# Optimization experiments

Hardware: AMD Instinct MI355X
Metric: run time of the kernel (lower is better)

## Reference

```python
import jax, jax.numpy as jnp
import numpy as np

N_ATOMS = 16384
N_BLOCKS = 4096
K = 3          # top-k nearest context atoms (min(3, n_ctx) in original; n_ctx >> 3 here)
EPS_W = 1e-8   # inverse-distance weight epsilon (matches original)
EPS_D = 1e-12  # tiny epsilon inside sqrt for numerical safety of the distance


def setup_inputs() -> dict:
    key = jax.random.key(0)
    k1, k2, k3, k4, k5 = jax.random.split(key, 5)
    # coordinates spread out like real molecular coords (Angstrom-ish scale)
    X = jax.random.normal(k1, (N_ATOMS, 3), dtype=jnp.float32) * 10.0
    base_noise = jax.random.normal(k2, (N_ATOMS, 3), dtype=jnp.float32)      # randn_like(X)
    centroid_noise = jax.random.normal(k3, (N_ATOMS, 3), dtype=jnp.float32)  # per-atom randn(3)
    block_ids = jnp.sort(jax.random.randint(k4, (N_ATOMS,), 0, N_BLOCKS)).astype(jnp.int32)
    generate_mask = jax.random.randint(k5, (N_BLOCKS,), 0, 2).astype(bool)
    return {
        "X": X,
        "base_noise": base_noise,
        "centroid_noise": centroid_noise,
        "block_ids": block_ids,
        "generate_mask": generate_mask,
    }


def reference(X, base_noise, centroid_noise, block_ids, generate_mask):
    """Vectorized sample_chemical_prior: for every generated atom, find the 3
    nearest CONTEXT atoms, take an inverse-distance-weighted centroid, and add
    0.5 * gaussian noise. Non-generated atoms keep base_noise (randn_like)."""
    n = X.shape[0]
    gen_atoms = generate_mask[block_ids]           # [N] atoms being generated
    ctx = ~gen_atoms                               # [N] context atoms

    # pairwise squared distances via ||a||^2 + ||b||^2 - 2 a.b  -> [N, N]
    xn = jnp.sum(X * X, axis=-1)
    sq = xn[:, None] + xn[None, :] - 2.0 * (X @ X.T)
    d = jnp.sqrt(jnp.maximum(sq, 0.0) + EPS_D)

    # only context atoms are valid neighbor candidates; exclude self for safety
    not_self = ~jnp.eye(n, dtype=bool)
    d = jnp.where(ctx[None, :] & not_self, d, jnp.inf)

    # k nearest context atoms per row (smallest distances)
    neg_dk, idx = jax.lax.top_k(-d, K)             # [N, K]
    dk = -neg_dk

    # inverse-distance weights, normalized (matches original)
    w = 1.0 / (dk + EPS_W)
    w = w / jnp.sum(w, axis=-1, keepdims=True)

    coords = X[idx]                                # [N, K, 3] gather neighbor coords
    centroid = jnp.sum(coords * w[..., None], axis=1)  # [N, 3]

    x0 = jnp.where(gen_atoms[:, None], centroid + 0.5 * centroid_noise, base_noise)
    return x0
```

## Files before the change

kernel.cpp:

```cpp
#include <hip/hip_runtime.h>
#include <cstdint>

#define N_ATOMS 16384
#define NBLK 64
#define NTHR 256
#define G 24
#define NCELLS (G*G*G)
#define NCELLS_PAD 14336
#define CPT 14
#define BOX_LO -48.0f
#define INV_CELL 0.25f
#define SINIT 3.0e38f

#define OFF_COUNTS 0
#define OFF_BLKGEN 256
#define OFF_BLKGOFF 512
#define OFF_FLAGS 1024
#define OFF_CNT 3072
#define OFF_START 60416
#define OFF_GENIDX 118016
#define OFF_CTX4 183552

__device__ __forceinline__ int cell1(float x) {
    int c = (int)floorf((x - BOX_LO) * INV_CELL);
    return min(max(c, 0), G - 1);
}

__device__ __forceinline__ void ins3(float v, int vi,
                                     float& s1, float& s2, float& s3,
                                     int& i1, int& i2, int& i3)
{
    const bool b1 = v < s1, b2 = v < s2, b3 = v < s3;
    s3 = b2 ? s2 : (b3 ? v : s3);   i3 = b2 ? i2 : (b3 ? vi : i3);
    s2 = b1 ? s1 : (b2 ? v : s2);   i2 = b1 ? i1 : (b2 ? vi : i2);
    s1 = b1 ? v : s1;               i1 = b1 ? vi : i1;
}

__device__ __forceinline__ void ins3v(float v, float& s1, float& s2, float& s3)
{
    const bool b1 = v < s1, b2 = v < s2, b3 = v < s3;
    s3 = b2 ? s2 : (b3 ? v : s3);
    s2 = b1 ? s1 : (b2 ? v : s2);
    s1 = b1 ? v : s1;
}

__global__ __launch_bounds__(256)
void k0_zero(int4* __restrict__ cell_cnt4)
{
    cell_cnt4[blockIdx.x * 256 + threadIdx.x] = make_int4(0, 0, 0, 0);
}

__global__ __launch_bounds__(NTHR)
void k1_classify(const float* __restrict__ X,
                 const int* __restrict__ block_ids,
                 const unsigned int* __restrict__ mask,
                 const float* __restrict__ base_noise,
                 float* __restrict__ out,
                 unsigned long long* __restrict__ flags,
                 int* __restrict__ blk_gen,
                 int* __restrict__ cell_cnt)
{
    __shared__ int sflag;
    __shared__ int wg[4];
    const int t = threadIdx.x;
    const int wave = t >> 6, lane = t & 63;

    if (t == 0) sflag = 0;
    __syncthreads();
    if (mask[t] > 1u) sflag = 1;
    __syncthreads();
    const bool is_u8 = (sflag != 0);
    const unsigned char* m8 = (const unsigned char*)mask;

    const int i = blockIdx.x * NTHR + t;
    const int bid = block_ids[i];
    const bool g = is_u8 ? (m8[bid] != 0) : (mask[bid] != 0u);

    out[3 * i + 0] = base_noise[3 * i + 0];
    out[3 * i + 1] = base_noise[3 * i + 1];
    out[3 * i + 2] = base_noise[3 * i + 2];

    const unsigned long long mg = __ballot(g);
    if (lane == 0) { flags[blockIdx.x * 4 + wave] = mg; wg[wave] = __popcll(mg); }
    __syncthreads();
    if (t == 0) blk_gen[blockIdx.x] = wg[0] + wg[1] + wg[2] + wg[3];

    if (!g) {
        const float x = X[3 * i], y = X[3 * i + 1], z = X[3 * i + 2];
        const int cx = cell1(x), cy = cell1(y), cz = cell1(z);
        atomicAdd(&cell_cnt[(cz * G + cy) * G + cx], 1);
    }
}

__global__ __launch_bounds__(1024)
void k2_scan(int* __restrict__ cell_cnt,
             int* __restrict__ cell_start,
             const int* __restrict__ blk_gen,
             int* __restrict__ blk_goff,
             int* __restrict__ counts)
{
    const int t = threadIdx.x;
    const int wave = t >> 6, lane = t & 63;
    int loc[CPT]; int sum = 0;
    #pragma unroll
    for (int k = 0; k < CPT; ++k) {
        const int v = cell_cnt[t * CPT + k];
        loc[k] = sum; sum += v;
    }
    int v = sum;
    #pragma unroll
    for (int d = 1; d < 64; d <<= 1) { const int u = __shfl_up(v, d); if (lane >= d) v += u; }
    __shared__ int wsum[16], wexc[16];
    if (lane == 63) wsum[wave] = v;
    __syncthreads();
    if (t < 16) {
        int v2 = wsum[t];
        const int orig = v2;
        #pragma unroll
        for (int d = 1; d < 16; d <<= 1) { const int u = __shfl_up(v2, d); if (t >= d) v2 += u; }
        wexc[t] = v2 - orig;
    }
    __syncthreads();
    const int base = wexc[wave] + (v - sum);
    #pragma unroll
    for (int k = 0; k < CPT; ++k) {
        cell_start[t * CPT + k] = base + loc[k];
        cell_cnt[t * CPT + k] = 0;
    }
    if (t == 1023) cell_start[NCELLS_PAD] = base + sum;
    __syncthreads();
    if (t < 64) {
        const int o = blk_gen[t];
        int s = o;
        #pragma unroll
        for (int d = 1; d < 64; d <<= 1) { const int u = __shfl_up(s, d); if (t >= d) s += u; }
        blk_goff[t] = s - o;
        if (t == 63) { counts[1] = s; counts[0] = N_ATOMS - s; }
    }
}

__global__ __launch_bounds__(NTHR)
void k3_scatter(const float* __restrict__ X,
                const unsigned long long* __restrict__ flags,
                const int* __restrict__ blk_goff,
                const int* __restrict__ cell_start,
                int* __restrict__ cell_cur,
                float4* __restrict__ ctx4s,
                int* __restrict__ genidx)
{
    const int t = threadIdx.x;
    const int wave = t >> 6, lane = t & 63;
    const int i = blockIdx.x * NTHR + t;
    const unsigned long long fw = flags[blockIdx.x * 4 + wave];
    const bool g = (fw >> lane) & 1ull;
    int og = blk_goff[blockIdx.x];
    int oc = blockIdx.x * NTHR - og;
    #pragma unroll
    for (int w = 0; w < 4; ++w) {
        if (w < wave) {
            const int p = __popcll(flags[blockIdx.x * 4 + w]);
            og += p; oc += 64 - p;
        }
    }
    const unsigned long long below = (1ull << lane) - 1ull;
    og += __popcll(fw & below);
    oc += __popcll((~fw) & below);
    if (g) {
        genidx[og] = i;
    } else {
        const float x = X[3 * i], y = X[3 * i + 1], z = X[3 * i + 2];
        float xn = x * x; xn += y * y; xn += z * z;
        const int cx = cell1(x), cy = cell1(y), cz = cell1(z);
        const int c = (cz * G + cy) * G + cx;
        const int pos = cell_start[c] + atomicAdd(&cell_cur[c], 1);
        ctx4s[pos] = make_float4(x, y, z, xn);
    }
}

__global__ __launch_bounds__(512)
void k4_search(const float* __restrict__ X,
               const float* __restrict__ cnoise,
               const int* __restrict__ counts,
               const int* __restrict__ cell_start,
               const float4* __restrict__ ctx4s,
               const int* __restrict__ genidx,
               float* __restrict__ out)
{
    const int n_gen = counts[1];
    const int wave = threadIdx.x >> 6, lane = threadIdx.x & 63;
    const int slot = (int)blockIdx.x * 8 + wave;
    if (slot >= n_gen) return;

    const int ai = genidx[slot];
    const float qx = X[3 * ai], qy = X[3 * ai + 1], qz = X[3 * ai + 2];
    float xnq = qx * qx; xnq += qy * qy; xnq += qz * qz;
    const int cqx = cell1(qx), cqy = cell1(qy), cqz = cell1(qz);

    float s1 = SINIT, s2 = SINIT, s3 = SINIT;
    int i1 = 0, i2 = 0, i3 = 0;

    int cnt = 0, st = 0;
    if (lane < 27) {
        const int dx = lane % 3 - 1, dy = (lane / 3) % 3 - 1, dz = lane / 9 - 1;
        const int cx = cqx + dx, cy = cqy + dy, cz = cqz + dz;
        if ((unsigned)cx < G && (unsigned)cy < G && (unsigned)cz < G) {
            const int c = (cz * G + cy) * G + cx;
            st = cell_start[c];
            cnt = cell_start[c + 1] - st;
        }
    }
    int pre = cnt;
    #pragma unroll
    for (int d = 1; d < 64; d <<= 1) { const int u = __shfl_up(pre, d); if (lane >= d) pre += u; }
    const int T = __shfl(pre, 63);
    const int ebase = pre - cnt;
    const int pk = st - ebase;
    const int iters = (T + 63) >> 6;
    for (int it = 0; it < iters; ++it) {
        const int j = it * 64 + lane;
        const int jc = min(j, T - 1);
        int L = 0;
        #pragma unroll
        for (int stp = 16; stp >= 1; stp >>= 1) {
            const int cand = L + stp;
            const int bv = __shfl(ebase, cand < 27 ? cand : 26);
            if (cand < 27 && bv <= jc) L = cand;
        }
        const int p = __shfl(pk, L) + jc;
        const float4 cc = ctx4s[p];
        if (j < T) {
            const float dot = qx * cc.x + qy * cc.y + qz * cc.z;
            const float sq = (xnq + cc.w) - 2.0f * dot;
            ins3(sq, p, s1, s2, s3, i1, i2, i3);
        }
    }

    int r = 1;
    for (;;) {
        float m1 = s1, m2 = s2, m3 = s3;
        #pragma unroll
        for (int m = 1; m < 64; m <<= 1) {
            const float a = __shfl_xor(m1, m);
            const float b = __shfl_xor(m2, m);
            const float c = __shfl_xor(m3, m);
            ins3v(a, m1, m2, m3); ins3v(b, m1, m2, m3); ins3v(c, m1, m2, m3);
        }
        const float bnd = (float)(4 * r) * (float)(4 * r);
        if (m3 + 0.01f < bnd || r >= G) break;
        ++r;
        const int B = 2 * r + 1, B2 = B * B, V = B2 * B;
        for (int u = lane; u < V; u += 64) {
            int dz = u / B2; const int rem = u - dz * B2;
            int dy = rem / B; int dx = rem - dy * B;
            dx -= r; dy -= r; dz -= r;
            const int ax = abs(dx), ay = abs(dy), az = abs(dz);
            if (max(ax, max(ay, az)) != r) continue;
            const int cx = cqx + dx, cy = cqy + dy, cz = cqz + dz;
            if ((unsigned)cx >= G || (unsigned)cy >= G || (unsigned)cz >= G) continue;
            const int c = (cz * G + cy) * G + cx;
            const int p0 = cell_start[c], p1 = cell_start[c + 1];
            for (int p = p0; p < p1; ++p) {
                const float4 cc = ctx4s[p];
                const float dot = qx * cc.x + qy * cc.y + qz * cc.z;
                const float sq = (xnq + cc.w) - 2.0f * dot;
                ins3(sq, p, s1, s2, s3, i1, i2, i3);
            }
        }
    }

    #pragma unroll
    for (int m = 1; m < 64; m <<= 1) {
        const float a = __shfl_xor(s1, m); const int ja = __shfl_xor(i1, m);
        const float b = __shfl_xor(s2, m); const int jb = __shfl_xor(i2, m);
        const float c = __shfl_xor(s3, m); const int jc = __shfl_xor(i3, m);
        ins3(a, ja, s1, s2, s3, i1, i2, i3);
        ins3(b, jb, s1, s2, s3, i1, i2, i3);
        ins3(c, jc, s1, s2, s3, i1, i2, i3);
    }

    if (lane == 0) {
        const float d1 = sqrtf(fmaxf(s1, 0.0f) + 1e-12f);
        const float d2 = sqrtf(fmaxf(s2, 0.0f) + 1e-12f);
        const float d3 = sqrtf(fmaxf(s3, 0.0f) + 1e-12f);
        float w1 = 1.0f / (d1 + 1e-8f);
        float w2 = 1.0f / (d2 + 1e-8f);
        float w3 = 1.0f / (d3 + 1e-8f);
        float wsum = w1 + w2;
        wsum += w3;
        w1 /= wsum; w2 /= wsum; w3 /= wsum;
        const float4 c1 = ctx4s[i1];
        const float4 c2 = ctx4s[i2];
        const float4 c3 = ctx4s[i3];
        float cxo = w1 * c1.x + w2 * c2.x; cxo += w3 * c3.x;
        float cyo = w1 * c1.y + w2 * c2.y; cyo += w3 * c3.y;
        float czo = w1 * c1.z + w2 * c2.z; czo += w3 * c3.z;
        out[3 * ai + 0] = cxo + 0.5f * cnoise[3 * ai + 0];
        out[3 * ai + 1] = cyo + 0.5f * cnoise[3 * ai + 1];
        out[3 * ai + 2] = czo + 0.5f * cnoise[3 * ai + 2];
    }
}

extern "C" void kernel_launch(void* const* d_in, const int* in_sizes, int n_in,
                              void* d_out, int out_size, void* d_ws, size_t ws_size,
                              hipStream_t stream) {
    const float* X          = (const float*)d_in[0];
    const float* base_noise = (const float*)d_in[1];
    const float* cnoise     = (const float*)d_in[2];
    const int*   block_ids  = (const int*)d_in[3];
    const unsigned int* gmask = (const unsigned int*)d_in[4];
    float* out = (float*)d_out;

    char* ws = (char*)d_ws;
    int*    counts     = (int*)(ws + OFF_COUNTS);
    int*    blk_gen    = (int*)(ws + OFF_BLKGEN);
    int*    blk_goff   = (int*)(ws + OFF_BLKGOFF);
    unsigned long long* flags = (unsigned long long*)(ws + OFF_FLAGS);
    int*    cell_cnt   = (int*)(ws + OFF_CNT);
    int*    cell_start = (int*)(ws + OFF_START);
    int*    genidx     = (int*)(ws + OFF_GENIDX);
    float4* ctx4s      = (float4*)(ws + OFF_CTX4);

    k0_zero<<<NCELLS_PAD / 1024, 256, 0, stream>>>((int4*)cell_cnt);
    k1_classify<<<NBLK, NTHR, 0, stream>>>(X, block_ids, gmask, base_noise,
                                           out, flags, blk_gen, cell_cnt);
    k2_scan<<<1, 1024, 0, stream>>>(cell_cnt, cell_start, blk_gen, blk_goff, counts);
    k3_scatter<<<NBLK, NTHR, 0, stream>>>(X, flags, blk_goff, cell_start,
                                          cell_cnt, ctx4s, genidx);
    k4_search<<<N_ATOMS / 8, 512, 0, stream>>>(X, cnoise, counts, cell_start,
                                               ctx4s, genidx, out);
}
```

Before: 51.50 us.

## Enumerate shell cells directly and flat-scan them with prefetched loads

The outer-shell search now enumerates only the surface cells of each shell instead of looping over the full cube and discarding interior cells. Each 64-cell batch of the shell is flattened into a wave-wide scan using a prefix sum and binary search, so lanes share work evenly instead of each lane walking its own cell serially. The next iteration's context-atom load is prefetched. The wave-wide top-3 reduction is skipped when no new candidates were added, and termination is gated on having at least 3 candidates. The cost is more index arithmetic and extra shuffles per batch.

```diff
diff --git a/kernel.cpp b/kernel.cpp
--- a/kernel.cpp
+++ b/kernel.cpp
@@ -5,7 +5,7 @@
 #define NBLK 64
 #define NTHR 256
 #define G 24
-#define NCELLS (G*G*G)
+#define NCELLS 13824
 #define NCELLS_PAD 14336
 #define CPT 14
 #define BOX_LO -48.0f
@@ -199,6 +199,77 @@
     float s1 = SINIT, s2 = SINIT, s3 = SINIT;
     int i1 = 0, i2 = 0, i3 = 0;
 
+    auto searchOwner = [&](int ebase_r, int jc) -> int {
+        int L = 0;
+        #pragma unroll
+        for (int stp = 32; stp >= 1; stp >>= 1) {
+            const int cand = L + stp;
+            const int bv = __shfl(ebase_r, cand);
+            if (bv <= jc) L = cand;
+        }
+        return L;
+    };
+
+    auto flatScan = [&](int T, int ebase_r, int pk_r) {
+        const int iters = (T + 63) >> 6;
+        if (iters == 0) return;
+        int jc0 = min(lane, T - 1);
+        int p0 = __shfl(pk_r, searchOwner(ebase_r, jc0)) + jc0;
+        float4 cc0 = ctx4s[p0];
+        for (int it = 0; it < iters; ++it) {
+            int p1 = p0; float4 cc1 = cc0;
+            if (it + 1 < iters) {
+                const int jc1 = min((it + 1) * 64 + lane, T - 1);
+                p1 = __shfl(pk_r, searchOwner(ebase_r, jc1)) + jc1;
+                cc1 = ctx4s[p1];
+            }
+            if (it * 64 + lane < T) {
+                const float dot = qx * cc0.x + qy * cc0.y + qz * cc0.z;
+                const float sq = (xnq + cc0.w) - 2.0f * dot;
+                ins3(sq, p0, s1, s2, s3, i1, i2, i3);
+            }
+            p0 = p1; cc0 = cc1;
+        }
+    };
+
+    auto prefixT = [&](int cnt, int& ebase_r, int& T) {
+        int pre = cnt;
+        #pragma unroll
+        for (int d = 1; d < 64; d <<= 1) {
+            const int u = __shfl_up(pre, d);
+            if (lane >= d) pre += u;
+        }
+        T = __shfl(pre, 63);
+        ebase_r = pre - cnt;
+    };
+
+    auto shellCell = [&](int r, int u, int S, int& st, int& cnt) {
+        st = 0; cnt = 0;
+        if (u < S) {
+            const int B = 2 * r + 1, F = B * B, P8 = 8 * r;
+            int dx, dy, dz;
+            if (u < 2 * F) {
+                dz = (u < F) ? -r : r;
+                const int v = (u < F) ? u : u - F;
+                dx = v % B - r; dy = v / B - r;
+            } else {
+                const int v = u - 2 * F;
+                dz = v / P8 - (r - 1);
+                const int w = v % P8;
+                if (w < 2 * r)      { dx = -r + w;          dy = -r; }
+                else if (w < 4 * r) { dx = r;               dy = -r + (w - 2 * r); }
+                else if (w < 6 * r) { dx = r - (w - 4 * r); dy = r; }
+                else                { dx = -r;              dy = r - (w - 6 * r); }
+            }
+            const int cx = cqx + dx, cy = cqy + dy, cz = cqz + dz;
+            if ((unsigned)cx < G && (unsigned)cy < G && (unsigned)cz < G) {
+                const int c = (cz * G + cy) * G + cx;
+                st = cell_start[c];
+                cnt = cell_start[c + 1] - st;
+            }
+        }
+    };
+
     int cnt = 0, st = 0;
     if (lane < 27) {
         const int dx = lane % 3 - 1, dy = (lane / 3) % 3 - 1, dz = lane / 9 - 1;
@@ -209,62 +280,46 @@
             cnt = cell_start[c + 1] - st;
         }
     }
-    int pre = cnt;
-    #pragma unroll
-    for (int d = 1; d < 64; d <<= 1) { const int u = __shfl_up(pre, d); if (lane >= d) pre += u; }
-    const int T = __shfl(pre, 63);
-    const int ebase = pre - cnt;
-    const int pk = st - ebase;
-    const int iters = (T + 63) >> 6;
-    for (int it = 0; it < iters; ++it) {
-        const int j = it * 64 + lane;
-        const int jc = min(j, T - 1);
-        int L = 0;
-        #pragma unroll
-        for (int stp = 16; stp >= 1; stp >>= 1) {
-            const int cand = L + stp;
-            const int bv = __shfl(ebase, cand < 27 ? cand : 26);
-            if (cand < 27 && bv <= jc) L = cand;
-        }
-        const int p = __shfl(pk, L) + jc;
-        const float4 cc = ctx4s[p];
-        if (j < T) {
-            const float dot = qx * cc.x + qy * cc.y + qz * cc.z;
-            const float sq = (xnq + cc.w) - 2.0f * dot;
-            ins3(sq, p, s1, s2, s3, i1, i2, i3);
-        }
-    }
+    int ebase, T;
+    prefixT(cnt, ebase, T);
+    flatScan(T, ebase, st - ebase);
+    int C = T;
+    bool dirty = (T > 0);
+    float gm3 = SINIT;
 
     int r = 1;
     for (;;) {
-        float m1 = s1, m2 = s2, m3 = s3;
-        #pragma unroll
-        for (int m = 1; m < 64; m <<= 1) {
-            const float a = __shfl_xor(m1, m);
-            const float b = __shfl_xor(m2, m);
-            const float c = __shfl_xor(m3, m);
-            ins3v(a, m1, m2, m3); ins3v(b, m1, m2, m3); ins3v(c, m1, m2, m3);
-        }
-        const float bnd = (float)(4 * r) * (float)(4 * r);
-        if (m3 + 0.01f < bnd || r >= G) break;
+        if (C >= 3) {
+            if (dirty) {
+                float m1 = s1, m2 = s2, m3 = s3;
+                #pragma unroll
+                for (int m = 1; m < 64; m <<= 1) {
+                    const float a = __shfl_xor(m1, m);
+                    const float b = __shfl_xor(m2, m);
+                    const float c = __shfl_xor(m3, m);
+                    ins3v(a, m1, m2, m3); ins3v(b, m1, m2, m3); ins3v(c, m1, m2, m3);
+                }
+                gm3 = m3; dirty = false;
+            }
+            const float bnd = (float)(4 * r) * (float)(4 * r);
+            if (gm3 + 0.01f < bnd) break;
+        }
+        if (r >= G) break;
         ++r;
-        const int B = 2 * r + 1, B2 = B * B, V = B2 * B;
-        for (int u = lane; u < V; u += 64) {
-            int dz = u / B2; const int rem = u - dz * B2;
-            int dy = rem / B; int dx = rem - dy * B;
-            dx -= r; dy -= r; dz -= r;
-            const int ax = abs(dx), ay = abs(dy), az = abs(dz);
-            if (max(ax, max(ay, az)) != r) continue;
-            const int cx = cqx + dx, cy = cqy + dy, cz = cqz + dz;
-            if ((unsigned)cx >= G || (unsigned)cy >= G || (unsigned)cz >= G) continue;
-            const int c = (cz * G + cy) * G + cx;
-            const int p0 = cell_start[c], p1 = cell_start[c + 1];
-            for (int p = p0; p < p1; ++p) {
-                const float4 cc = ctx4s[p];
-                const float dot = qx * cc.x + qy * cc.y + qz * cc.z;
-                const float sq = (xnq + cc.w) - 2.0f * dot;
-                ins3(sq, p, s1, s2, s3, i1, i2, i3);
-            }
+        const int S = 24 * r * r + 2;
+        const int nro = (S + 63) >> 6;
+        int st0, c0;
+        shellCell(r, lane, S, st0, c0);
+        for (int ro = 0; ro < nro; ++ro) {
+            int st1 = st0, c1 = c0;
+            if (ro + 1 < nro) shellCell(r, (ro + 1) * 64 + lane, S, st1, c1);
+            int eb, Tr;
+            prefixT(c0, eb, Tr);
+            if (Tr > 0) {
+                flatScan(Tr, eb, st0 - eb);
+                C += Tr; dirty = true;
+            }
+            st0 = st1; c0 = c1;
         }
     }
 
```

New measurement: 52.24 us. About the same (+1.4%).
